# Optimization experiments

Hardware: AMD Instinct MI355X
Metric: run time of the kernel (lower is better)

The kernel has to match this reference:

```python
import jax, jax.numpy as jnp
import numpy as np

N, D = 8192, 256
E = 65536


def setup_inputs() -> dict:
    key = jax.random.key(0)
    ks = jax.random.split(key, 16)
    s = 1.0 / np.sqrt(D)  # nn.Linear default init scale
    return {
        "x_mean": jax.random.normal(ks[0], (N, D), dtype=jnp.float32),
        "x_var": jax.random.uniform(ks[1], (N, D), dtype=jnp.float32),
        "edge_index": jax.random.randint(ks[2], (2, E), 0, N, dtype=jnp.int64),
        "edge_timestamps": jax.random.uniform(ks[3], (E,), dtype=jnp.float32),
        "Wq": jax.random.uniform(ks[4], (D, D), jnp.float32, -s, s),
        "bq": jax.random.uniform(ks[5], (D,), jnp.float32, -s, s),
        "Wk": jax.random.uniform(ks[6], (D, D), jnp.float32, -s, s),
        "bk": jax.random.uniform(ks[7], (D,), jnp.float32, -s, s),
        "Wv": jax.random.uniform(ks[8], (D, D), jnp.float32, -s, s),
        "bv": jax.random.uniform(ks[9], (D,), jnp.float32, -s, s),
        "Wo": jax.random.uniform(ks[10], (D, D), jnp.float32, -s, s),
        "bo": jax.random.uniform(ks[11], (D,), jnp.float32, -s, s),
        "Wvar": jax.random.uniform(ks[12], (D, D), jnp.float32, -s, s),
        "bvar": jax.random.uniform(ks[13], (D,), jnp.float32, -s, s),
    }


def reference(x_mean, x_var, edge_index, edge_timestamps,
              Wq, bq, Wk, bk, Wv, bv, Wo, bo, Wvar, bvar):
    # edge_index / edge_timestamps are accepted but unused (as in the original forward).
    head_dim = D // 4  # num_heads=4; heads are never split, only used for scale
    scale = head_dim ** -0.5

    q = x_mean @ Wq.T + bq  # [N, D]
    k = x_mean @ Wk.T + bk
    v = x_mean @ Wv.T + bv

    attn = jax.nn.softmax((q @ k.T) * scale, axis=-1)  # [N, N] (dropout: eval mode)

    out_mean = (attn @ v) @ Wo.T + bo  # [N, D]

    v_var = x_var @ Wvar.T + bvar
    out_var = (attn * attn) @ v_var  # squared weights against projected variance
    return out_mean, out_var
```

## Files before the change

### kernel.cpp

```cpp
#include <hip/hip_runtime.h>
#include <hip/hip_bf16.h>
#include <hip/hip_fp16.h>

#define DEV __device__ __forceinline__

typedef __attribute__((ext_vector_type(8))) _Float16 h8;
typedef __attribute__((ext_vector_type(4))) float floatx4;

DEV float bf2f(unsigned short b) { return __uint_as_float(((unsigned)b) << 16); }

DEV void async_ld16(const void* g, void* l) {
  __builtin_amdgcn_global_load_lds(
      (const __attribute__((address_space(1))) unsigned int*)g,
      (__attribute__((address_space(3))) unsigned int*)l, 16, 0, 0);
}

DEV size_t fl_idx(size_t i, size_t j, int tpc) {
  return ((i >> 4) * (size_t)tpc + (j >> 5)) * 512 +
         (((i & 15) + ((j >> 3) & 3) * 16) * 8) + (j & 7);
}

DEV int detect_bf16(const void* x_mean) {
  const unsigned* w = (const unsigned*)x_mean;
  unsigned v = w[threadIdx.x & 63];
  unsigned ex = (v >> 7) & 0xFFu;
  int vote = (ex >= 100u && ex <= 144u) ? 1 : 0;
  unsigned long long b = __ballot(vote);
  return __popcll(b) >= 48 ? 1 : 0;
}

DEV float load_elem(const void* p, int isbf, size_t i) {
  return isbf ? bf2f(((const unsigned short*)p)[i]) : ((const float*)p)[i];
}

DEV void stage8h(const void* src, int isbf, size_t idx, float scale, _Float16* dst) {
  h8 o;
  if (isbf) {
    const unsigned short* s = (const unsigned short*)src + idx;
#pragma unroll
    for (int j = 0; j < 8; ++j) o[j] = (_Float16)(bf2f(s[j]) * scale);
  } else {
    const float* f = (const float*)src + idx;
    float4 a = *(const float4*)f;
    float4 b = *(const float4*)(f + 4);
    o[0] = (_Float16)(a.x * scale); o[1] = (_Float16)(a.y * scale);
    o[2] = (_Float16)(a.z * scale); o[3] = (_Float16)(a.w * scale);
    o[4] = (_Float16)(b.x * scale); o[5] = (_Float16)(b.y * scale);
    o[6] = (_Float16)(b.z * scale); o[7] = (_Float16)(b.w * scale);
  }
  *(h8*)dst = o;
}

template <bool F32_OUT>
DEV void gemm_cvt_core(const void* A, int a_bf, const void* B, int b_bf,
                       const void* bias, int bias_bf, const float* rowdiv,
                       void* __restrict__ Cv, size_t ldc, int fl_tpc,
                       size_t i0, size_t j0, float scale, int bias_mode) {
  __shared__ __align__(16) _Float16 As[128 * 32];
  __shared__ __align__(16) _Float16 Bs[128 * 32];
  const int t = threadIdx.x;
  const int lane = t & 63, wave = t >> 6;
  const int wr = wave >> 1, wc = wave & 1;
  const int q = lane >> 4, m = lane & 15;
  floatx4 acc[4][4] = {};
  for (int k0 = 0; k0 < 256; k0 += 32) {
#pragma unroll
    for (int it = 0; it < 2; ++it) {
      int e = it * 2048 + t * 8;
      int row = e >> 5, col = e & 31;
      float asc = rowdiv ? 1.f / rowdiv[i0 + row] : 1.f;
      stage8h(A, a_bf, (i0 + row) * (size_t)256 + k0 + col, asc, &As[e]);
      stage8h(B, b_bf, (j0 + row) * (size_t)256 + k0 + col, 1.f, &Bs[e]);
    }
    __syncthreads();
    h8 af[4], bfr[4];
#pragma unroll
    for (int r = 0; r < 4; ++r)
      af[r] = *(const h8*)&As[(wr * 64 + r * 16 + m) * 32 + q * 8];
#pragma unroll
    for (int c = 0; c < 4; ++c)
      bfr[c] = *(const h8*)&Bs[(wc * 64 + c * 16 + m) * 32 + q * 8];
#pragma unroll
    for (int r = 0; r < 4; ++r)
#pragma unroll
      for (int c = 0; c < 4; ++c)
        acc[r][c] = __builtin_amdgcn_mfma_f32_16x16x32_f16(af[r], bfr[c], acc[r][c], 0, 0, 0);
    __syncthreads();
  }
#pragma unroll
  for (int r = 0; r < 4; ++r) {
#pragma unroll
    for (int c = 0; c < 4; ++c) {
      size_t col = j0 + wc * 64 + c * 16 + m;
      float bcol = (bias_mode == 0) ? load_elem(bias, bias_bf, col) : 0.f;
#pragma unroll
      for (int g = 0; g < 4; ++g) {
        size_t row = i0 + wr * 64 + r * 16 + q * 4 + g;
        float val = acc[r][c][g] + bcol;
        if (bias_mode == 1) val += load_elem(bias, bias_bf, row);
        val *= scale;
        if (F32_OUT)
          ((float*)Cv)[row * ldc + col] = val;
        else if (fl_tpc > 0)
          ((_Float16*)Cv)[fl_idx(row, col, fl_tpc)] = (_Float16)val;
        else
          ((_Float16*)Cv)[row * ldc + col] = (_Float16)val;
      }
    }
  }
}

struct ProjArgs {
  const void* A[4];
  const void* B[4];
  const void* bias[4];
  _Float16* C[4];
  int fl_tpc[4];
  float scale[4];
  int bias_row[4];
  const void* xdet;
};

__global__ __launch_bounds__(256) void proj_kernel(ProjArgs p) {
  int isbf = detect_bf16(p.xdet);
  int z = blockIdx.z;
  size_t i0, j0;
  if (z < 2) { i0 = (size_t)blockIdx.x * 128; j0 = (size_t)blockIdx.y * 128; }
  else       { i0 = (size_t)blockIdx.y * 128; j0 = (size_t)blockIdx.x * 128; }
  gemm_cvt_core<false>(p.A[z], isbf, p.B[z], isbf, p.bias[z], isbf, nullptr,
                       p.C[z], 0, p.fl_tpc[z], i0, j0, p.scale[z], p.bias_row[z]);
}

__global__ __launch_bounds__(256) void qk_exp_kernel(const _Float16* __restrict__ qb,
                                                     const _Float16* __restrict__ kb,
                                                     _Float16* __restrict__ E,
                                                     float* __restrict__ rs) {
  __shared__ __align__(16) char smem[128 * 136 * 2];
  _Float16* As = (_Float16*)smem;
  _Float16* Bs = As + 4096;
  _Float16* Ts = (_Float16*)smem;
  const int t = threadIdx.x;
  const int lane = t & 63, wave = t >> 6;
  const int wr = wave >> 1, wc = wave & 1;
  const int q = lane >> 4, m = lane & 15;
  const size_t bx = blockIdx.x, by = blockIdx.y;
  const size_t i0 = bx * 128, j0 = by * 128;
  floatx4 acc[4][4] = {};
  for (int kt = 0; kt < 8; ++kt) {
#pragma unroll
    for (int it = 0; it < 2; ++it) {
      int c = it * 4 + wave;
      async_ld16(&qb[((bx * 8 + c) * 8 + kt) * 512 + lane * 8], &As[c * 512 + lane * 8]);
      async_ld16(&kb[((by * 8 + c) * 8 + kt) * 512 + lane * 8], &Bs[c * 512 + lane * 8]);
    }
    __syncthreads();
    h8 af[4], bfr[4];
#pragma unroll
    for (int r = 0; r < 4; ++r)
      af[r] = *(const h8*)&As[(wr * 4 + r) * 512 + lane * 8];
#pragma unroll
    for (int c = 0; c < 4; ++c)
      bfr[c] = *(const h8*)&Bs[(wc * 4 + c) * 512 + lane * 8];
#pragma unroll
    for (int r = 0; r < 4; ++r)
#pragma unroll
      for (int c = 0; c < 4; ++c)
        acc[r][c] = __builtin_amdgcn_mfma_f32_16x16x32_f16(af[r], bfr[c], acc[r][c], 0, 0, 0);
    __syncthreads();
  }
#pragma unroll
  for (int r = 0; r < 4; ++r)
#pragma unroll
    for (int c = 0; c < 4; ++c)
#pragma unroll
      for (int g = 0; g < 4; ++g)
        acc[r][c][g] = __expf(fminf(acc[r][c][g], 8.f)) * 0.015625f;
#pragma unroll
  for (int r = 0; r < 4; ++r)
#pragma unroll
    for (int g = 0; g < 4; ++g) {
      float part = acc[r][0][g] + acc[r][1][g] + acc[r][2][g] + acc[r][3][g];
      part += __shfl_xor(part, 1);
      part += __shfl_xor(part, 2);
      part += __shfl_xor(part, 4);
      part += __shfl_xor(part, 8);
      if (m == 0)
        unsafeAtomicAdd(&rs[i0 + wr * 64 + r * 16 + q * 4 + g], part);
    }
#pragma unroll
  for (int r = 0; r < 4; ++r)
#pragma unroll
    for (int c = 0; c < 4; ++c)
#pragma unroll
      for (int g = 0; g < 4; ++g)
        Ts[(wr * 64 + r * 16 + q * 4 + g) * 136 + wc * 64 + c * 16 + m] =
            (_Float16)acc[r][c][g];
  __syncthreads();
#pragma unroll
  for (int it = 0; it < 8; ++it) {
    int cch = it * 4 + wave;
    int ci = cch >> 2, ck = cch & 3;
    int il = ci * 16 + (lane & 15);
    int jl = ck * 32 + (lane >> 4) * 8;
    h8 v = *(const h8*)&Ts[il * 136 + jl];
    *(h8*)&E[((bx * 8 + ci) * 256 + by * 4 + ck) * 512 + lane * 8] = v;
  }
}

__global__ __launch_bounds__(256) void zero_rs_kernel(float* __restrict__ rs) {
  rs[blockIdx.x * 256 + threadIdx.x] = 0.f;
}
__global__ __launch_bounds__(256) void zero_acc_kernel(float* __restrict__ a,
                                                       float* __restrict__ b) {
  size_t i = ((size_t)blockIdx.x * 256 + threadIdx.x) * 4;
  float4 z = {0.f, 0.f, 0.f, 0.f};
  *(float4*)(a + i) = z;
  *(float4*)(b + i) = z;
}

__global__ __launch_bounds__(256) void av_fused(const _Float16* __restrict__ E,
                                                const _Float16* __restrict__ vT,
                                                const _Float16* __restrict__ vvT,
                                                float* __restrict__ otm,
                                                float* __restrict__ otv) {
  __shared__ __align__(16) _Float16 As[4 * 512];
  __shared__ __align__(16) _Float16 B1s[8 * 512];
  __shared__ __align__(16) _Float16 B2s[8 * 512];
  const int t = threadIdx.x;
  const int lane = t & 63, wave = t >> 6;
  const int wr = wave >> 1, wc = wave & 1;
  const int q = lane >> 4, m = lane & 15;
  const size_t bx = blockIdx.x, by = blockIdx.y;
  const int kt0 = (blockIdx.z == 0) ? 0 : 86 + (blockIdx.z - 1) * 85;
  const int ktn = (blockIdx.z == 0) ? 86 : 85;
  floatx4 accm[2][4] = {}, accv[2][4] = {};
  for (int kk = 0; kk < ktn; ++kk) {
    int kt = kt0 + kk;
    async_ld16(&E[((bx * 4 + wave) * 256 + kt) * 512 + lane * 8],
               &As[wave * 512 + lane * 8]);
#pragma unroll
    for (int it = 0; it < 2; ++it) {
      int c = it * 4 + wave;
      async_ld16(&vT[((by * 8 + c) * 256 + kt) * 512 + lane * 8],
                 &B1s[c * 512 + lane * 8]);
      async_ld16(&vvT[((by * 8 + c) * 256 + kt) * 512 + lane * 8],
                 &B2s[c * 512 + lane * 8]);
    }
    __syncthreads();
    h8 a[2], a2[2], b1[4], b2[4];
#pragma unroll
    for (int r = 0; r < 2; ++r) {
      a[r] = *(const h8*)&As[(wr * 2 + r) * 512 + lane * 8];
      a2[r] = a[r] * a[r];
    }
#pragma unroll
    for (int c = 0; c < 4; ++c) {
      b1[c] = *(const h8*)&B1s[(wc * 4 + c) * 512 + lane * 8];
      b2[c] = *(const h8*)&B2s[(wc * 4 + c) * 512 + lane * 8];
    }
#pragma unroll
    for (int r = 0; r < 2; ++r)
#pragma unroll
      for (int c = 0; c < 4; ++c) {
        accm[r][c] = __builtin_amdgcn_mfma_f32_16x16x32_f16(a[r], b1[c], accm[r][c], 0, 0, 0);
        accv[r][c] = __builtin_amdgcn_mfma_f32_16x16x32_f16(a2[r], b2[c], accv[r][c], 0, 0, 0);
      }
    __syncthreads();
  }
#pragma unroll
  for (int r = 0; r < 2; ++r)
#pragma unroll
    for (int c = 0; c < 4; ++c) {
      size_t col = by * 128 + wc * 64 + c * 16 + m;
#pragma unroll
      for (int g = 0; g < 4; ++g) {
        size_t row = bx * 64 + wr * 32 + r * 16 + q * 4 + g;
        unsafeAtomicAdd(&otm[row * 256 + col], accm[r][c][g]);
        unsafeAtomicAdd(&otv[row * 256 + col], accv[r][c][g]);
      }
    }
}

__global__ __launch_bounds__(256) void var_div_kernel(float* __restrict__ ov,
                                                      const float* __restrict__ rs) {
  size_t i = ((size_t)blockIdx.x * 256 + threadIdx.x) * 4;
  float inv = 1.f / rs[i >> 8];
  float s = inv * inv;
  float4 v = *(float4*)(ov + i);
  v.x *= s; v.y *= s; v.z *= s; v.w *= s;
  *(float4*)(ov + i) = v;
}

__global__ __launch_bounds__(256) void final_kernel(const float* __restrict__ ot,
                                                    const void* Wo, const void* bo,
                                                    const float* __restrict__ rs,
                                                    const void* xdet,
                                                    float* __restrict__ Cm) {
  int isbf = detect_bf16(xdet);
  gemm_cvt_core<true>(ot, 0, Wo, isbf, bo, isbf, rs, Cm, 256, 0,
                      (size_t)blockIdx.x * 128, (size_t)blockIdx.y * 128, 1.f, 0);
}

extern "C" void kernel_launch(void* const* d_in, const int* in_sizes, int n_in,
                              void* d_out, int out_size, void* d_ws, size_t ws_size,
                              hipStream_t stream) {
  const void* x_mean = d_in[0];
  const void* x_var  = d_in[1];
  const void* Wq   = d_in[4];
  const void* bq   = d_in[5];
  const void* Wk   = d_in[6];
  const void* bk   = d_in[7];
  const void* Wv   = d_in[8];
  const void* bv   = d_in[9];
  const void* Wo   = d_in[10];
  const void* bo   = d_in[11];
  const void* Wvar = d_in[12];
  const void* bvar = d_in[13];
  float* out = (float*)d_out;

  const size_t NE_S = 67108864;
  const size_t NE_P = 2097152;
  if (ws_size < (NE_S + 5 * NE_P) * 2) return;
  _Float16* w   = (_Float16*)d_ws;
  _Float16* S   = w;
  _Float16* qb  = w + NE_S;
  _Float16* kb  = qb + NE_P;
  _Float16* vT  = kb + NE_P;
  _Float16* vvT = vT + NE_P;
  float* rs     = (float*)(vvT + NE_P);
  float* ot_f32 = (float*)qb;

  ProjArgs p;
  p.A[0] = x_mean; p.B[0] = Wq;     p.bias[0] = bq;   p.C[0] = qb;  p.fl_tpc[0] = 8;   p.scale[0] = 0.125f; p.bias_row[0] = 0;
  p.A[1] = x_mean; p.B[1] = Wk;     p.bias[1] = bk;   p.C[1] = kb;  p.fl_tpc[1] = 8;   p.scale[1] = 1.f;    p.bias_row[1] = 0;
  p.A[2] = Wv;     p.B[2] = x_mean; p.bias[2] = bv;   p.C[2] = vT;  p.fl_tpc[2] = 256; p.scale[2] = 1.f;    p.bias_row[2] = 1;
  p.A[3] = Wvar;   p.B[3] = x_var;  p.bias[3] = bvar; p.C[3] = vvT; p.fl_tpc[3] = 256; p.scale[3] = 1.f;    p.bias_row[3] = 1;
  p.xdet = x_mean;

  zero_rs_kernel<<<dim3(32), 256, 0, stream>>>(rs);
  proj_kernel<<<dim3(64, 2, 4), 256, 0, stream>>>(p);
  qk_exp_kernel<<<dim3(64, 64), 256, 0, stream>>>(qb, kb, S, rs);
  zero_acc_kernel<<<dim3(2048), 256, 0, stream>>>(ot_f32, out + NE_P);
  av_fused<<<dim3(128, 2, 3), 256, 0, stream>>>(S, vT, vvT, ot_f32, out + NE_P);
  var_div_kernel<<<dim3(2048), 256, 0, stream>>>(out + NE_P, rs);
  final_kernel<<<dim3(64, 2), 256, 0, stream>>>(ot_f32, Wo, bo, rs, x_mean, out);
}
```

Before: 351.5 us.

## Split fused attention-value kernel into two 128x128-tile passes over E

The fused kernel that computed attn@v and attn^2@v_var together with 64x128 tiles is replaced by a templated kernel run twice, once per output, using 128x128 tiles and a 6-way split-K. Each pass uses half the LDS of the fused version and precomputes load offsets, which raises arithmetic intensity per tile and may improve occupancy. The cost is that the large E matrix is read twice from memory instead of once, and there are more atomic partial sums because of the 6-way split.

```diff
diff --git a/kernel.cpp b/kernel.cpp
--- a/kernel.cpp
+++ b/kernel.cpp
@@ -144,7 +144,7 @@
   const int wr = wave >> 1, wc = wave & 1;
   const int q = lane >> 4, m = lane & 15;
   const size_t bx = blockIdx.x, by = blockIdx.y;
-  const size_t i0 = bx * 128, j0 = by * 128;
+  const size_t i0 = bx * 128;
   floatx4 acc[4][4] = {};
   for (int kt = 0; kt < 8; ++kt) {
 #pragma unroll
@@ -218,65 +218,62 @@
   *(float4*)(b + i) = z;
 }
 
-__global__ __launch_bounds__(256) void av_fused(const _Float16* __restrict__ E,
-                                                const _Float16* __restrict__ vT,
-                                                const _Float16* __restrict__ vvT,
-                                                float* __restrict__ otm,
-                                                float* __restrict__ otv) {
-  __shared__ __align__(16) _Float16 As[4 * 512];
-  __shared__ __align__(16) _Float16 B1s[8 * 512];
-  __shared__ __align__(16) _Float16 B2s[8 * 512];
+template <bool SQ>
+__global__ __launch_bounds__(256) void av_core(const _Float16* __restrict__ E,
+                                               const _Float16* __restrict__ BT,
+                                               float* __restrict__ outp) {
+  __shared__ __align__(16) _Float16 As[4096];
+  __shared__ __align__(16) _Float16 Bs[4096];
   const int t = threadIdx.x;
   const int lane = t & 63, wave = t >> 6;
   const int wr = wave >> 1, wc = wave & 1;
   const int q = lane >> 4, m = lane & 15;
   const size_t bx = blockIdx.x, by = blockIdx.y;
-  const int kt0 = (blockIdx.z == 0) ? 0 : 86 + (blockIdx.z - 1) * 85;
-  const int ktn = (blockIdx.z == 0) ? 86 : 85;
-  floatx4 accm[2][4] = {}, accv[2][4] = {};
-  for (int kk = 0; kk < ktn; ++kk) {
-    int kt = kt0 + kk;
-    async_ld16(&E[((bx * 4 + wave) * 256 + kt) * 512 + lane * 8],
-               &As[wave * 512 + lane * 8]);
+  const int z = blockIdx.z;
+  const int s0 = z * 43;
+  const int sn = (z == 5) ? 41 : 43;
+  size_t aoff[2], boff[2];
+#pragma unroll
+  for (int it = 0; it < 2; ++it) {
+    int n = it * 256 + t;
+    aoff[it] = ((bx * 8 + (size_t)(n >> 6)) * 256 + (size_t)s0) * 512 + (n & 63) * 8;
+    boff[it] = ((by * 8 + (size_t)(n >> 6)) * 256 + (size_t)s0) * 512 + (n & 63) * 8;
+  }
+  floatx4 acc[4][4] = {};
+  for (int kk = 0; kk < sn; ++kk) {
 #pragma unroll
     for (int it = 0; it < 2; ++it) {
-      int c = it * 4 + wave;
-      async_ld16(&vT[((by * 8 + c) * 256 + kt) * 512 + lane * 8],
-                 &B1s[c * 512 + lane * 8]);
-      async_ld16(&vvT[((by * 8 + c) * 256 + kt) * 512 + lane * 8],
-                 &B2s[c * 512 + lane * 8]);
-    }
-    __syncthreads();
-    h8 a[2], a2[2], b1[4], b2[4];
-#pragma unroll
-    for (int r = 0; r < 2; ++r) {
-      a[r] = *(const h8*)&As[(wr * 2 + r) * 512 + lane * 8];
-      a2[r] = a[r] * a[r];
-    }
-#pragma unroll
-    for (int c = 0; c < 4; ++c) {
-      b1[c] = *(const h8*)&B1s[(wc * 4 + c) * 512 + lane * 8];
-      b2[c] = *(const h8*)&B2s[(wc * 4 + c) * 512 + lane * 8];
-    }
-#pragma unroll
-    for (int r = 0; r < 2; ++r)
-#pragma unroll
-      for (int c = 0; c < 4; ++c) {
-        accm[r][c] = __builtin_amdgcn_mfma_f32_16x16x32_f16(a[r], b1[c], accm[r][c], 0, 0, 0);
-        accv[r][c] = __builtin_amdgcn_mfma_f32_16x16x32_f16(a2[r], b2[c], accv[r][c], 0, 0, 0);
-      }
-    __syncthreads();
-  }
-#pragma unroll
-  for (int r = 0; r < 2; ++r)
+      async_ld16(&E[aoff[it]], &As[(it * 256 + t) * 8]);
+      async_ld16(&BT[boff[it]], &Bs[(it * 256 + t) * 8]);
+    }
+    __syncthreads();
+    h8 af[4], bfr[4];
+#pragma unroll
+    for (int r = 0; r < 4; ++r) {
+      af[r] = *(const h8*)&As[(wr * 4 + r) * 512 + lane * 8];
+      if (SQ) af[r] = af[r] * af[r];
+    }
+#pragma unroll
+    for (int c = 0; c < 4; ++c)
+      bfr[c] = *(const h8*)&Bs[(wc * 4 + c) * 512 + lane * 8];
+#pragma unroll
+    for (int r = 0; r < 4; ++r)
+#pragma unroll
+      for (int c = 0; c < 4; ++c)
+        acc[r][c] = __builtin_amdgcn_mfma_f32_16x16x32_f16(af[r], bfr[c], acc[r][c], 0, 0, 0);
+    __syncthreads();
+#pragma unroll
+    for (int it = 0; it < 2; ++it) { aoff[it] += 512; boff[it] += 512; }
+  }
+#pragma unroll
+  for (int r = 0; r < 4; ++r)
 #pragma unroll
     for (int c = 0; c < 4; ++c) {
       size_t col = by * 128 + wc * 64 + c * 16 + m;
 #pragma unroll
       for (int g = 0; g < 4; ++g) {
-        size_t row = bx * 64 + wr * 32 + r * 16 + q * 4 + g;
-        unsafeAtomicAdd(&otm[row * 256 + col], accm[r][c][g]);
-        unsafeAtomicAdd(&otv[row * 256 + col], accv[r][c][g]);
+        size_t row = bx * 128 + wr * 64 + r * 16 + q * 4 + g;
+        unsafeAtomicAdd(&outp[row * 256 + col], acc[r][c][g]);
       }
     }
 }
@@ -341,7 +338,8 @@
   proj_kernel<<<dim3(64, 2, 4), 256, 0, stream>>>(p);
   qk_exp_kernel<<<dim3(64, 64), 256, 0, stream>>>(qb, kb, S, rs);
   zero_acc_kernel<<<dim3(2048), 256, 0, stream>>>(ot_f32, out + NE_P);
-  av_fused<<<dim3(128, 2, 3), 256, 0, stream>>>(S, vT, vvT, ot_f32, out + NE_P);
+  av_core<false><<<dim3(64, 2, 6), 256, 0, stream>>>(S, vT, ot_f32);
+  av_core<true><<<dim3(64, 2, 6), 256, 0, stream>>>(S, vvT, out + NE_P);
   var_div_kernel<<<dim3(2048), 256, 0, stream>>>(out + NE_P, rs);
   final_kernel<<<dim3(64, 2), 256, 0, stream>>>(ot_f32, Wo, bo, rs, x_mean, out);
 }
```

Result: slower. 387.2 us (+10.2%).

## Fold row normalization into AV epilogue, drop var_div kernel, retile projection and output GEMMs

Applied to the files above, without the earlier changes.

The softmax row-sum division (and its square for the variance path) now happens in the av_fused epilogue before the atomic adds, so the separate var_div kernel and the per-row divide in the final GEMM are gone. The projection kernel now stages its output tile through LDS and writes the fragment-layout buffers with coalesced 16-byte stores instead of scattered half-precision stores. The final output GEMM uses 64-row tiles to launch twice as many blocks. av_fused also precomputes pointer offsets and gets an occupancy hint. The cost is more multiplies inside the atomic epilogue, which runs once per split-K slice.

```diff
diff --git a/kernel.cpp b/kernel.cpp
--- a/kernel.cpp
+++ b/kernel.cpp
@@ -13,11 +13,6 @@
   __builtin_amdgcn_global_load_lds(
       (const __attribute__((address_space(1))) unsigned int*)g,
       (__attribute__((address_space(3))) unsigned int*)l, 16, 0, 0);
-}
-
-DEV size_t fl_idx(size_t i, size_t j, int tpc) {
-  return ((i >> 4) * (size_t)tpc + (j >> 5)) * 512 +
-         (((i & 15) + ((j >> 3) & 3) * 16) * 8) + (j & 7);
 }
 
 DEV int detect_bf16(const void* x_mean) {
@@ -49,65 +44,6 @@
     o[6] = (_Float16)(b.z * scale); o[7] = (_Float16)(b.w * scale);
   }
   *(h8*)dst = o;
-}
-
-template <bool F32_OUT>
-DEV void gemm_cvt_core(const void* A, int a_bf, const void* B, int b_bf,
-                       const void* bias, int bias_bf, const float* rowdiv,
-                       void* __restrict__ Cv, size_t ldc, int fl_tpc,
-                       size_t i0, size_t j0, float scale, int bias_mode) {
-  __shared__ __align__(16) _Float16 As[128 * 32];
-  __shared__ __align__(16) _Float16 Bs[128 * 32];
-  const int t = threadIdx.x;
-  const int lane = t & 63, wave = t >> 6;
-  const int wr = wave >> 1, wc = wave & 1;
-  const int q = lane >> 4, m = lane & 15;
-  floatx4 acc[4][4] = {};
-  for (int k0 = 0; k0 < 256; k0 += 32) {
-#pragma unroll
-    for (int it = 0; it < 2; ++it) {
-      int e = it * 2048 + t * 8;
-      int row = e >> 5, col = e & 31;
-      float asc = rowdiv ? 1.f / rowdiv[i0 + row] : 1.f;
-      stage8h(A, a_bf, (i0 + row) * (size_t)256 + k0 + col, asc, &As[e]);
-      stage8h(B, b_bf, (j0 + row) * (size_t)256 + k0 + col, 1.f, &Bs[e]);
-    }
-    __syncthreads();
-    h8 af[4], bfr[4];
-#pragma unroll
-    for (int r = 0; r < 4; ++r)
-      af[r] = *(const h8*)&As[(wr * 64 + r * 16 + m) * 32 + q * 8];
-#pragma unroll
-    for (int c = 0; c < 4; ++c)
-      bfr[c] = *(const h8*)&Bs[(wc * 64 + c * 16 + m) * 32 + q * 8];
-#pragma unroll
-    for (int r = 0; r < 4; ++r)
-#pragma unroll
-      for (int c = 0; c < 4; ++c)
-        acc[r][c] = __builtin_amdgcn_mfma_f32_16x16x32_f16(af[r], bfr[c], acc[r][c], 0, 0, 0);
-    __syncthreads();
-  }
-#pragma unroll
-  for (int r = 0; r < 4; ++r) {
-#pragma unroll
-    for (int c = 0; c < 4; ++c) {
-      size_t col = j0 + wc * 64 + c * 16 + m;
-      float bcol = (bias_mode == 0) ? load_elem(bias, bias_bf, col) : 0.f;
-#pragma unroll
-      for (int g = 0; g < 4; ++g) {
-        size_t row = i0 + wr * 64 + r * 16 + q * 4 + g;
-        float val = acc[r][c][g] + bcol;
-        if (bias_mode == 1) val += load_elem(bias, bias_bf, row);
-        val *= scale;
-        if (F32_OUT)
-          ((float*)Cv)[row * ldc + col] = val;
-        else if (fl_tpc > 0)
-          ((_Float16*)Cv)[fl_idx(row, col, fl_tpc)] = (_Float16)val;
-        else
-          ((_Float16*)Cv)[row * ldc + col] = (_Float16)val;
-      }
-    }
-  }
 }
 
 struct ProjArgs {
@@ -122,13 +58,76 @@
 };
 
 __global__ __launch_bounds__(256) void proj_kernel(ProjArgs p) {
+  __shared__ __align__(16) char smem[34816];
+  _Float16* As = (_Float16*)smem;
+  _Float16* Bs = As + 4096;
+  _Float16* Ts = (_Float16*)smem;
   int isbf = detect_bf16(p.xdet);
   int z = blockIdx.z;
   size_t i0, j0;
   if (z < 2) { i0 = (size_t)blockIdx.x * 128; j0 = (size_t)blockIdx.y * 128; }
   else       { i0 = (size_t)blockIdx.y * 128; j0 = (size_t)blockIdx.x * 128; }
-  gemm_cvt_core<false>(p.A[z], isbf, p.B[z], isbf, p.bias[z], isbf, nullptr,
-                       p.C[z], 0, p.fl_tpc[z], i0, j0, p.scale[z], p.bias_row[z]);
+  const void* A = p.A[z];
+  const void* B = p.B[z];
+  const void* bias = p.bias[z];
+  const float scale = p.scale[z];
+  const int bias_row = p.bias_row[z];
+  const int tpc = p.fl_tpc[z];
+  _Float16* C = p.C[z];
+  const int t = threadIdx.x;
+  const int lane = t & 63, wave = t >> 6;
+  const int wr = wave >> 1, wc = wave & 1;
+  const int q = lane >> 4, m = lane & 15;
+  floatx4 acc[4][4] = {};
+  for (int k0 = 0; k0 < 256; k0 += 32) {
+#pragma unroll
+    for (int it = 0; it < 2; ++it) {
+      int e = it * 2048 + t * 8;
+      int row = e >> 5, col = e & 31;
+      stage8h(A, isbf, (i0 + row) * (size_t)256 + k0 + col, 1.f, &As[e]);
+      stage8h(B, isbf, (j0 + row) * (size_t)256 + k0 + col, 1.f, &Bs[e]);
+    }
+    __syncthreads();
+    h8 af[4], bfr[4];
+#pragma unroll
+    for (int r = 0; r < 4; ++r)
+      af[r] = *(const h8*)&As[(wr * 64 + r * 16 + m) * 32 + q * 8];
+#pragma unroll
+    for (int c = 0; c < 4; ++c)
+      bfr[c] = *(const h8*)&Bs[(wc * 64 + c * 16 + m) * 32 + q * 8];
+#pragma unroll
+    for (int r = 0; r < 4; ++r)
+#pragma unroll
+      for (int c = 0; c < 4; ++c)
+        acc[r][c] = __builtin_amdgcn_mfma_f32_16x16x32_f16(af[r], bfr[c], acc[r][c], 0, 0, 0);
+    __syncthreads();
+  }
+#pragma unroll
+  for (int r = 0; r < 4; ++r)
+#pragma unroll
+    for (int c = 0; c < 4; ++c) {
+      size_t col = j0 + wc * 64 + c * 16 + m;
+      float bcol = bias_row ? 0.f : load_elem(bias, isbf, col);
+#pragma unroll
+      for (int g = 0; g < 4; ++g) {
+        size_t row = i0 + wr * 64 + r * 16 + q * 4 + g;
+        float val = acc[r][c][g] + bcol;
+        if (bias_row) val += load_elem(bias, isbf, row);
+        Ts[(wr * 64 + r * 16 + q * 4 + g) * 136 + wc * 64 + c * 16 + m] =
+            (_Float16)(val * scale);
+      }
+    }
+  __syncthreads();
+  size_t ti0 = i0 >> 4, tj0 = j0 >> 5;
+#pragma unroll
+  for (int it = 0; it < 8; ++it) {
+    int cch = it * 4 + wave;
+    int ci = cch >> 2, ck = cch & 3;
+    int il = ci * 16 + (lane & 15);
+    int jl = ck * 32 + (lane >> 4) * 8;
+    h8 v = *(const h8*)&Ts[il * 136 + jl];
+    *(h8*)&C[((ti0 + ci) * (size_t)tpc + (tj0 + ck)) * 512 + lane * 8] = v;
+  }
 }
 
 __global__ __launch_bounds__(256) void qk_exp_kernel(const _Float16* __restrict__ qb,
@@ -144,7 +143,7 @@
   const int wr = wave >> 1, wc = wave & 1;
   const int q = lane >> 4, m = lane & 15;
   const size_t bx = blockIdx.x, by = blockIdx.y;
-  const size_t i0 = bx * 128, j0 = by * 128;
+  const size_t i0 = bx * 128;
   floatx4 acc[4][4] = {};
   for (int kt = 0; kt < 8; ++kt) {
 #pragma unroll
@@ -218,11 +217,12 @@
   *(float4*)(b + i) = z;
 }
 
-__global__ __launch_bounds__(256) void av_fused(const _Float16* __restrict__ E,
-                                                const _Float16* __restrict__ vT,
-                                                const _Float16* __restrict__ vvT,
-                                                float* __restrict__ otm,
-                                                float* __restrict__ otv) {
+__global__ __launch_bounds__(256, 4) void av_fused(const _Float16* __restrict__ E,
+                                                   const _Float16* __restrict__ vT,
+                                                   const _Float16* __restrict__ vvT,
+                                                   const float* __restrict__ rs,
+                                                   float* __restrict__ otm,
+                                                   float* __restrict__ otv) {
   __shared__ __align__(16) _Float16 As[4 * 512];
   __shared__ __align__(16) _Float16 B1s[8 * 512];
   __shared__ __align__(16) _Float16 B2s[8 * 512];
@@ -233,19 +233,16 @@
   const size_t bx = blockIdx.x, by = blockIdx.y;
   const int kt0 = (blockIdx.z == 0) ? 0 : 86 + (blockIdx.z - 1) * 85;
   const int ktn = (blockIdx.z == 0) ? 86 : 85;
+  size_t aoff = ((bx * 4 + (size_t)wave) * 256 + (size_t)kt0) * 512 + lane * 8;
+  size_t boff0 = ((by * 8 + (size_t)wave) * 256 + (size_t)kt0) * 512 + lane * 8;
+  size_t boff1 = ((by * 8 + (size_t)wave + 4) * 256 + (size_t)kt0) * 512 + lane * 8;
   floatx4 accm[2][4] = {}, accv[2][4] = {};
   for (int kk = 0; kk < ktn; ++kk) {
-    int kt = kt0 + kk;
-    async_ld16(&E[((bx * 4 + wave) * 256 + kt) * 512 + lane * 8],
-               &As[wave * 512 + lane * 8]);
-#pragma unroll
-    for (int it = 0; it < 2; ++it) {
-      int c = it * 4 + wave;
-      async_ld16(&vT[((by * 8 + c) * 256 + kt) * 512 + lane * 8],
-                 &B1s[c * 512 + lane * 8]);
-      async_ld16(&vvT[((by * 8 + c) * 256 + kt) * 512 + lane * 8],
-                 &B2s[c * 512 + lane * 8]);
-    }
+    async_ld16(&E[aoff], &As[wave * 512 + lane * 8]);
+    async_ld16(&vT[boff0], &B1s[wave * 512 + lane * 8]);
+    async_ld16(&vT[boff1], &B1s[(wave + 4) * 512 + lane * 8]);
+    async_ld16(&vvT[boff0], &B2s[wave * 512 + lane * 8]);
+    async_ld16(&vvT[boff1], &B2s[(wave + 4) * 512 + lane * 8]);
     __syncthreads();
     h8 a[2], a2[2], b1[4], b2[4];
 #pragma unroll
@@ -266,39 +263,76 @@
         accv[r][c] = __builtin_amdgcn_mfma_f32_16x16x32_f16(a2[r], b2[c], accv[r][c], 0, 0, 0);
       }
     __syncthreads();
+    aoff += 512; boff0 += 512; boff1 += 512;
   }
 #pragma unroll
   for (int r = 0; r < 2; ++r)
 #pragma unroll
-    for (int c = 0; c < 4; ++c) {
-      size_t col = by * 128 + wc * 64 + c * 16 + m;
-#pragma unroll
-      for (int g = 0; g < 4; ++g) {
-        size_t row = bx * 64 + wr * 32 + r * 16 + q * 4 + g;
-        unsafeAtomicAdd(&otm[row * 256 + col], accm[r][c][g]);
-        unsafeAtomicAdd(&otv[row * 256 + col], accv[r][c][g]);
+    for (int g = 0; g < 4; ++g) {
+      size_t row = bx * 64 + wr * 32 + r * 16 + q * 4 + g;
+      float inv = 1.f / rs[row];
+      float inv2 = inv * inv;
+#pragma unroll
+      for (int c = 0; c < 4; ++c) {
+        size_t col = by * 128 + wc * 64 + c * 16 + m;
+        unsafeAtomicAdd(&otm[row * 256 + col], accm[r][c][g] * inv);
+        unsafeAtomicAdd(&otv[row * 256 + col], accv[r][c][g] * inv2);
       }
     }
-}
-
-__global__ __launch_bounds__(256) void var_div_kernel(float* __restrict__ ov,
-                                                      const float* __restrict__ rs) {
-  size_t i = ((size_t)blockIdx.x * 256 + threadIdx.x) * 4;
-  float inv = 1.f / rs[i >> 8];
-  float s = inv * inv;
-  float4 v = *(float4*)(ov + i);
-  v.x *= s; v.y *= s; v.z *= s; v.w *= s;
-  *(float4*)(ov + i) = v;
 }
 
 __global__ __launch_bounds__(256) void final_kernel(const float* __restrict__ ot,
                                                     const void* Wo, const void* bo,
-                                                    const float* __restrict__ rs,
                                                     const void* xdet,
                                                     float* __restrict__ Cm) {
+  __shared__ __align__(16) _Float16 As[64 * 32];
+  __shared__ __align__(16) _Float16 Bs[128 * 32];
   int isbf = detect_bf16(xdet);
-  gemm_cvt_core<true>(ot, 0, Wo, isbf, bo, isbf, rs, Cm, 256, 0,
-                      (size_t)blockIdx.x * 128, (size_t)blockIdx.y * 128, 1.f, 0);
+  const int t = threadIdx.x;
+  const int lane = t & 63, wave = t >> 6;
+  const int wr = wave >> 1, wc = wave & 1;
+  const int q = lane >> 4, m = lane & 15;
+  const size_t i0 = (size_t)blockIdx.x * 64, j0 = (size_t)blockIdx.y * 128;
+  floatx4 acc[2][4] = {};
+  for (int k0 = 0; k0 < 256; k0 += 32) {
+    {
+      int e = t * 8;
+      int row = e >> 5, col = e & 31;
+      stage8h(ot, 0, (i0 + row) * (size_t)256 + k0 + col, 1.f, &As[e]);
+    }
+#pragma unroll
+    for (int it = 0; it < 2; ++it) {
+      int e = it * 2048 + t * 8;
+      int row = e >> 5, col = e & 31;
+      stage8h(Wo, isbf, (j0 + row) * (size_t)256 + k0 + col, 1.f, &Bs[e]);
+    }
+    __syncthreads();
+    h8 af[2], bfr[4];
+#pragma unroll
+    for (int r = 0; r < 2; ++r)
+      af[r] = *(const h8*)&As[(wr * 32 + r * 16 + m) * 32 + q * 8];
+#pragma unroll
+    for (int c = 0; c < 4; ++c)
+      bfr[c] = *(const h8*)&Bs[(wc * 64 + c * 16 + m) * 32 + q * 8];
+#pragma unroll
+    for (int r = 0; r < 2; ++r)
+#pragma unroll
+      for (int c = 0; c < 4; ++c)
+        acc[r][c] = __builtin_amdgcn_mfma_f32_16x16x32_f16(af[r], bfr[c], acc[r][c], 0, 0, 0);
+    __syncthreads();
+  }
+#pragma unroll
+  for (int r = 0; r < 2; ++r)
+#pragma unroll
+    for (int c = 0; c < 4; ++c) {
+      size_t col = j0 + wc * 64 + c * 16 + m;
+      float bcol = load_elem(bo, isbf, col);
+#pragma unroll
+      for (int g = 0; g < 4; ++g) {
+        size_t row = i0 + wr * 32 + r * 16 + q * 4 + g;
+        Cm[row * 256 + col] = acc[r][c][g] + bcol;
+      }
+    }
 }
 
 extern "C" void kernel_launch(void* const* d_in, const int* in_sizes, int n_in,
@@ -341,7 +375,6 @@
   proj_kernel<<<dim3(64, 2, 4), 256, 0, stream>>>(p);
   qk_exp_kernel<<<dim3(64, 64), 256, 0, stream>>>(qb, kb, S, rs);
   zero_acc_kernel<<<dim3(2048), 256, 0, stream>>>(ot_f32, out + NE_P);
-  av_fused<<<dim3(128, 2, 3), 256, 0, stream>>>(S, vT, vvT, ot_f32, out + NE_P);
-  var_div_kernel<<<dim3(2048), 256, 0, stream>>>(out + NE_P, rs);
-  final_kernel<<<dim3(64, 2), 256, 0, stream>>>(ot_f32, Wo, bo, rs, x_mean, out);
-}
+  av_fused<<<dim3(128, 2, 3), 256, 0, stream>>>(S, vT, vvT, rs, ot_f32, out + NE_P);
+  final_kernel<<<dim3(128, 2), 256, 0, stream>>>(ot_f32, Wo, bo, x_mean, out);
+}
```

Result: faster. 322.4 us (-8.3%).
